# Kernel optimization log

Hardware: AMD Instinct MI355X
Metric: run time of the kernel (lower is better)

The kernel has to match this reference:

```python
import jax, jax.numpy as jnp
import numpy as np

N, DEG, D_IN, D_HID = 50000, 16, 963, 256


def setup_inputs() -> dict:
    key = jax.random.key(0)
    ks = jax.random.split(key, 8)
    s = 0.02
    neighbours = jax.random.randint(ks[0], (N, DEG), 0, N)
    shape_features = jax.random.normal(ks[1], (N, D_IN), dtype=jnp.float32)
    # layer 0: D_IN -> D_HID; layers 1..13 (stacked): D_HID -> D_HID; extra: D_HID -> 3
    W_self0 = jax.random.normal(ks[2], (D_IN, D_HID), dtype=jnp.float32) * s
    W_neigh0 = jax.random.normal(ks[3], (D_IN, D_HID), dtype=jnp.float32) * s
    b0 = jnp.zeros((D_HID,), jnp.float32)
    W_self = jax.random.normal(ks[4], (13, D_HID, D_HID), dtype=jnp.float32) * s
    W_neigh = jax.random.normal(ks[5], (13, D_HID, D_HID), dtype=jnp.float32) * s
    b = jnp.zeros((13, D_HID), jnp.float32)
    W_extra = jax.random.normal(ks[6], (D_HID, 3), dtype=jnp.float32) * s
    b_extra = jnp.zeros((3,), jnp.float32)
    return {
        "neighbours": neighbours,
        "shape_features": shape_features,
        "W_self0": W_self0, "W_neigh0": W_neigh0, "b0": b0,
        "W_self": W_self, "W_neigh": W_neigh, "b": b,
        "W_extra": W_extra, "b_extra": b_extra,
    }


def _gcn(x, neighbours, Ws, Wn, bias):
    # gather neighbour features [N, DEG, D] and sum-aggregate, plus self transform
    agg = jnp.take(x, neighbours, axis=0).sum(axis=1)
    return x @ Ws + agg @ Wn + bias


def reference(neighbours, shape_features, W_self0, W_neigh0, b0, W_self, W_neigh, b, W_extra, b_extra):
    x = jax.nn.relu(_gcn(shape_features, neighbours, W_self0, W_neigh0, b0))
    for i in range(6):  # 6 residual blocks of 2 GCN layers each
        temp = x
        x = jax.nn.relu(_gcn(x, neighbours, W_self[2 * i], W_neigh[2 * i], b[2 * i]))
        x = jax.nn.relu(_gcn(x, neighbours, W_self[2 * i + 1], W_neigh[2 * i + 1], b[2 * i + 1]))
        x = (temp + x) / 2
    x = jax.nn.relu(_gcn(x, neighbours, W_self[12], W_neigh[12], b[12]))
    coordinates = x @ W_extra + b_extra  # extra layer called without neighbours -> linear
    return (x, coordinates)
```

## Files before the change

### kernel.cpp

```cpp
#include <hip/hip_runtime.h>
#include <hip/hip_bf16.h>
#include <hip/hip_fp16.h>
#include <stdint.h>

#define NNODES 50000
#define NPAD   50048
#define DEG    16
#define DIN    963
#define K0PAD  992
#define DHID   256
#define SCALE  (1.0f / 1024.0f)
#define ISCALE 1024.0f

typedef __attribute__((ext_vector_type(4))) float    f32x4;
typedef __attribute__((ext_vector_type(8))) _Float16 f16x8;
typedef __attribute__((ext_vector_type(4))) _Float16 f16x4;

typedef const __attribute__((address_space(1))) void GV;
typedef __attribute__((address_space(3))) void LV;

__device__ __forceinline__ void gl2lds16(const void* g, void* l) {
    __builtin_amdgcn_global_load_lds((GV*)g, (LV*)l, 16, 0, 0);
}

__global__ __launch_bounds__(256) void gemm_dual0(
    const _Float16* __restrict__ A, int K,
    const _Float16* __restrict__ Wp,
    _Float16* __restrict__ ys, _Float16* __restrict__ yn)
{
    __shared__ _Float16 lds[2][2][4096];

    const int tid  = threadIdx.x;
    const int w    = tid >> 6;
    const int lane = tid & 63;
    const int bm   = blockIdx.x * 128;
    const int nb   = blockIdx.y * 128;

    const int KT = K >> 5;

    auto stage = [&](int s, int kt) {
        const int k0 = kt << 5;
#pragma unroll
        for (int i = 0; i < 2; ++i) {
            const int j   = w + (i << 2);
            const int c   = (j << 6) + lane;
            const int row = c & 127;
            const int k8  = (c >> 7) << 3;
            gl2lds16(A  + (size_t)(bm + row) * K + k0 + k8, &lds[s][0][(size_t)j << 9]);
            gl2lds16(Wp + (size_t)(nb + row) * K + k0 + k8, &lds[s][1][(size_t)j << 9]);
        }
    };

    const int wm = (w >> 1) << 6;
    const int wn = (w & 1) << 6;
    const int lr = lane & 15;
    const int kh = lane >> 4;

    f32x4 acc[4][4] = {};

    stage(0, 0);
    __syncthreads();
    int cur = 0;
    for (int kt = 0; kt < KT; ++kt) {
        if (kt + 1 < KT) stage(cur ^ 1, kt + 1);
        f16x8 a[4], b[4];
#pragma unroll
        for (int mi = 0; mi < 4; ++mi)
            a[mi] = *(const f16x8*)&lds[cur][0][((kh << 7) + wm + (mi << 4) + lr) << 3];
#pragma unroll
        for (int ni = 0; ni < 4; ++ni)
            b[ni] = *(const f16x8*)&lds[cur][1][((kh << 7) + wn + (ni << 4) + lr) << 3];
#pragma unroll
        for (int mi = 0; mi < 4; ++mi)
#pragma unroll
            for (int ni = 0; ni < 4; ++ni)
                acc[mi][ni] = __builtin_amdgcn_mfma_f32_16x16x32_f16(a[mi], b[ni], acc[mi][ni], 0, 0, 0);
        __syncthreads();
        cur ^= 1;
    }

    _Float16* C = (blockIdx.y < 2) ? ys : yn;
    const int cb = (nb & 255) + wn;
#pragma unroll
    for (int mi = 0; mi < 4; ++mi) {
        const size_t rbase = (size_t)(bm + wm + (mi << 4) + (kh << 2)) << 8;
#pragma unroll
        for (int ni = 0; ni < 4; ++ni) {
            const int col = cb + (ni << 4) + lr;
#pragma unroll
            for (int r = 0; r < 4; ++r)
                C[rbase + ((size_t)r << 8) + col] = (_Float16)acc[mi][ni][r];
        }
    }
}

template<int FINAL>
__global__ __launch_bounds__(512) void fused_layer(
    const _Float16* __restrict__ X, const int* __restrict__ nbr,
    const _Float16* __restrict__ W, const float* __restrict__ bias,
    const _Float16* __restrict__ res,
    _Float16* __restrict__ outh, float* __restrict__ outf)
{
    __shared__ _Float16 ldsA[2][4096];
    __shared__ _Float16 ldsB[2][8192];

    const int tid  = threadIdx.x;
    const int w    = tid >> 6;
    const int lane = tid & 63;
    const int bm   = blockIdx.x << 7;

    const int growg = bm + (tid >> 2);
    const int nrow  = (growg < NNODES) ? growg : (NNODES - 1);
    const int4* np  = (const int4*)(nbr + nrow * DEG);
    const int4 q0 = np[0], q1 = np[1], q2 = np[2], q3 = np[3];
    const int kq = (tid & 3) << 3;

    auto GLD = [&](int r, int ko) -> f16x8 {
        return *(const f16x8*)(X + ((size_t)r << 8) + ko);
    };
    auto stageAself = [&](int s, int kt) {
        const int c = tid;
        gl2lds16(X + ((size_t)(bm + (c & 127)) << 8) + (kt << 5) + ((c >> 7) << 3),
                 &ldsA[s][(size_t)c << 3]);
    };
    auto stageB = [&](int s, int kt) {
#pragma unroll
        for (int i = 0; i < 2; ++i) {
            const int c = (i << 9) + tid;
            gl2lds16(W + ((size_t)(c & 255) << 9) + (kt << 5) + ((c >> 8) << 3),
                     &ldsB[s][(size_t)c << 3]);
        }
    };

    const int wm = (w >> 2) << 6;
    const int wn = (w & 3) << 6;
    const int lr = lane & 15;
    const int kh = lane >> 4;

    f32x4 acc[4][4] = {};
    f16x8 g0, g1, g2, g3, g4, g5, g6, g7;

    stageAself(0, 0);
    stageB(0, 0);
    __syncthreads();

    int cur = 0;
#pragma unroll
    for (int kt = 0; kt < 16; ++kt) {
        const int nxt = kt + 1;
        if (nxt < 16) {
            if (nxt < 8) {
                stageAself(cur ^ 1, nxt);
            } else {
                const int ko = ((nxt - 8) << 5) + kq;
                g0 = GLD(q0.x, ko); g1 = GLD(q0.y, ko); g2 = GLD(q0.z, ko); g3 = GLD(q0.w, ko);
                g4 = GLD(q1.x, ko); g5 = GLD(q1.y, ko); g6 = GLD(q1.z, ko); g7 = GLD(q1.w, ko);
            }
            stageB(cur ^ 1, nxt);
        }
        f16x8 a[4], b[4];
#pragma unroll
        for (int mi = 0; mi < 4; ++mi)
            a[mi] = *(const f16x8*)&ldsA[cur][((kh << 7) + wm + (mi << 4) + lr) << 3];
#pragma unroll
        for (int ni = 0; ni < 4; ++ni)
            b[ni] = *(const f16x8*)&ldsB[cur][((kh << 8) + wn + (ni << 4) + lr) << 3];
#pragma unroll
        for (int mi = 0; mi < 4; ++mi)
#pragma unroll
            for (int ni = 0; ni < 4; ++ni)
                acc[mi][ni] = __builtin_amdgcn_mfma_f32_16x16x32_f16(a[mi], b[ni], acc[mi][ni], 0, 0, 0);
        if (nxt >= 8 && nxt < 16) {
            const int ko = ((nxt - 8) << 5) + kq;
            f16x8 s0 = ((g0 + g1) + (g2 + g3)) + ((g4 + g5) + (g6 + g7));
            g0 = GLD(q2.x, ko); g1 = GLD(q2.y, ko); g2 = GLD(q2.z, ko); g3 = GLD(q2.w, ko);
            g4 = GLD(q3.x, ko); g5 = GLD(q3.y, ko); g6 = GLD(q3.z, ko); g7 = GLD(q3.w, ko);
            f16x8 s1 = ((g0 + g1) + (g2 + g3)) + ((g4 + g5) + (g6 + g7));
            *(f16x8*)&ldsA[cur ^ 1][(size_t)(((tid & 3) << 7) + (tid >> 2)) << 3] = s0 + s1;
        }
        __syncthreads();
        cur ^= 1;
    }

    const int r0 = kh << 2;
#pragma unroll
    for (int mi = 0; mi < 4; ++mi) {
        const int grow0 = bm + wm + (mi << 4) + r0;
#pragma unroll
        for (int ni = 0; ni < 4; ++ni) {
            const int col = wn + (ni << 4) + lr;
            const float bcol = bias[col] * SCALE;
#pragma unroll
            for (int r = 0; r < 4; ++r) {
                const int grow = grow0 + r;
                float s = acc[mi][ni][r] + bcol;
                s = fmaxf(s, 0.f);
                if (res) s = ((float)res[((size_t)grow << 8) + col] + s) * 0.5f;
                if (FINAL) {
                    if (grow < NNODES) outf[((size_t)grow << 8) + col] = s * ISCALE;
                } else {
                    outh[((size_t)grow << 8) + col] = (_Float16)s;
                }
            }
        }
    }
}

__global__ __launch_bounds__(256) void combine0(
    const _Float16* __restrict__ ys, const _Float16* __restrict__ yn,
    const int* __restrict__ nbr, const float* __restrict__ bias,
    _Float16* __restrict__ outh)
{
    const int w    = threadIdx.x >> 6;
    const int lane = threadIdx.x & 63;
    const int n    = (blockIdx.x << 2) + w;
    const int c4   = lane << 2;
    const size_t base = ((size_t)n << 8) + c4;

    const f16x4 ysv = *(const f16x4*)(ys + base);
    const float4 bv = *(const float4*)(bias + c4);
    float s0 = (float)ysv[0] + bv.x * SCALE;
    float s1 = (float)ysv[1] + bv.y * SCALE;
    float s2 = (float)ysv[2] + bv.z * SCALE;
    float s3 = (float)ysv[3] + bv.w * SCALE;

    const int* nr = nbr + n * DEG;
#pragma unroll
    for (int j = 0; j < DEG; ++j) {
        const f16x4 v = *(const f16x4*)(yn + (((size_t)nr[j]) << 8) + c4);
        s0 += (float)v[0]; s1 += (float)v[1]; s2 += (float)v[2]; s3 += (float)v[3];
    }
    f16x4 o;
    o[0] = (_Float16)fmaxf(s0, 0.f); o[1] = (_Float16)fmaxf(s1, 0.f);
    o[2] = (_Float16)fmaxf(s2, 0.f); o[3] = (_Float16)fmaxf(s3, 0.f);
    *(f16x4*)(outh + base) = o;
}

__global__ __launch_bounds__(64) void coords_kernel(
    const float* __restrict__ x, const float* __restrict__ We,
    const float* __restrict__ be, float* __restrict__ out3, int N)
{
    const int n = blockIdx.x;
    const int l = threadIdx.x;
    const float4 xv = *(const float4*)(x + (size_t)n * 256 + l * 4);
    float p0 = 0.f, p1 = 0.f, p2 = 0.f;
    const float xs[4] = {xv.x, xv.y, xv.z, xv.w};
#pragma unroll
    for (int i = 0; i < 4; ++i) {
        const int cidx = l * 4 + i;
        p0 += xs[i] * We[cidx * 3 + 0];
        p1 += xs[i] * We[cidx * 3 + 1];
        p2 += xs[i] * We[cidx * 3 + 2];
    }
#pragma unroll
    for (int off = 32; off > 0; off >>= 1) {
        p0 += __shfl_down(p0, off);
        p1 += __shfl_down(p1, off);
        p2 += __shfl_down(p2, off);
    }
    if (l == 0) {
        out3[(size_t)n * 3 + 0] = p0 + be[0];
        out3[(size_t)n * 3 + 1] = p1 + be[1];
        out3[(size_t)n * 3 + 2] = p2 + be[2];
    }
}

__global__ __launch_bounds__(256) void conv_sf(const float* __restrict__ sf,
                                               _Float16* __restrict__ sfb)
{
    const int idx = blockIdx.x * 256 + threadIdx.x;
    const int row = idx / 124;
    const int k8  = (idx % 124) << 3;
    f16x8 o = {};
    if (row < NNODES) {
#pragma unroll
        for (int i = 0; i < 8; ++i) {
            const int k = k8 + i;
            o[i] = (k < DIN) ? (_Float16)(sf[(size_t)row * DIN + k] * SCALE) : (_Float16)0.f;
        }
    }
    *(f16x8*)(sfb + (size_t)row * K0PAD + k8) = o;
}

__global__ __launch_bounds__(256) void pack_w0(const float* __restrict__ Ws0,
                                               const float* __restrict__ Wn0,
                                               _Float16* __restrict__ Wp0)
{
    const int idx = blockIdx.x * 256 + threadIdx.x;
    const int nn  = idx & 511;
    const int k8  = idx >> 9;
    const float* W = (nn < 256) ? Ws0 : Wn0;
    const int n0 = nn & 255;
    f16x8 o;
#pragma unroll
    for (int i = 0; i < 8; ++i) {
        const int k = (k8 << 3) + i;
        o[i] = (k < DIN) ? (_Float16)W[(size_t)k * 256 + n0] : (_Float16)0.f;
    }
    *(f16x8*)(Wp0 + (size_t)nn * K0PAD + (k8 << 3)) = o;
}

__global__ __launch_bounds__(256) void pack_w2(const float* __restrict__ Ws,
                                               const float* __restrict__ Wn,
                                               _Float16* __restrict__ Wpk2)
{
    const int idx = blockIdx.x * 256 + threadIdx.x;
    const int n   = idx & 255;
    const int k8  = (idx >> 8) & 63;
    const int l   = idx >> 14;
    f16x8 o;
#pragma unroll
    for (int i = 0; i < 8; ++i) {
        const int k = (k8 << 3) + i;
        const float* W = (k < 256) ? Ws : Wn;
        o[i] = (_Float16)W[(size_t)l * 65536 + (k & 255) * 256 + n];
    }
    *(f16x8*)(Wpk2 + (size_t)l * 131072 + (size_t)n * 512 + (k8 << 3)) = o;
}

extern "C" void kernel_launch(void* const* d_in, const int* in_sizes, int n_in,
                              void* d_out, int out_size, void* d_ws, size_t ws_size,
                              hipStream_t stream)
{
    const int*   nbr = (const int*)d_in[0];
    const float* sf  = (const float*)d_in[1];
    const float* Ws0 = (const float*)d_in[2];
    const float* Wn0 = (const float*)d_in[3];
    const float* b0  = (const float*)d_in[4];
    const float* Ws  = (const float*)d_in[5];
    const float* Wn  = (const float*)d_in[6];
    const float* bb  = (const float*)d_in[7];
    const float* We  = (const float*)d_in[8];
    const float* be  = (const float*)d_in[9];
    float* out = (float*)d_out;

    uint8_t* w = (uint8_t*)d_ws;
    _Float16* sfb  = (_Float16*)w;
    _Float16* P    = (_Float16*)w;
    _Float16* Q    = P + (size_t)NPAD * 256;
    _Float16* Wpk2 = Q + (size_t)NPAD * 256;
    _Float16* Wp0  = (_Float16*)(w + (size_t)NPAD * K0PAD * 2);
    _Float16* ysb  = Wp0 + (size_t)512 * K0PAD;
    _Float16* ynb  = ysb + (size_t)NPAD * 256;

    conv_sf<<<NPAD * 124 / 256, 256, 0, stream>>>(sf, sfb);
    pack_w0<<<512 * 124 / 256, 256, 0, stream>>>(Ws0, Wn0, Wp0);

    gemm_dual0<<<dim3(NPAD / 128, 4), 256, 0, stream>>>(sfb, K0PAD, Wp0, ysb, ynb);
    pack_w2<<<13 * 64 * 256 / 256, 256, 0, stream>>>(Ws, Wn, Wpk2);
    combine0<<<NNODES / 4, 256, 0, stream>>>(ysb, ynb, nbr, b0, P);

    const int fg = NPAD / 128;

    for (int t = 0; t < 6; ++t) {
        const int lA = 2 * t, lB = lA + 1;
        fused_layer<0><<<fg, 512, 0, stream>>>(P, nbr, Wpk2 + (size_t)lA * 131072,
                                               bb + lA * 256, nullptr, Q, nullptr);
        fused_layer<0><<<fg, 512, 0, stream>>>(Q, nbr, Wpk2 + (size_t)lB * 131072,
                                               bb + lB * 256, P, P, nullptr);
    }

    fused_layer<1><<<fg, 512, 0, stream>>>(P, nbr, Wpk2 + (size_t)12 * 131072,
                                           bb + 12 * 256, nullptr, nullptr, out);

    coords_kernel<<<NNODES, 64, 0, stream>>>(out, We, be, out + (size_t)NNODES * 256, NNODES);
}
```

Measured before the change: 1.588 ms.

## Vectorize GEMM epilogues via swapped MFMA operands, XCD-swizzle blocks, widen combine loads

The MFMA operands are swapped so each lane holds four consecutive output columns, which lets the GEMM and fused-layer epilogues do vector f16x4/float4 stores and residual and bias loads instead of scalar ones. The layer-0 GEMM grid is flattened and remapped with an XCD-aware swizzle so neighbouring tiles that share the same A rows land on the same chiplet's L2. The combine kernel now has each thread handle 8 columns with all 16 neighbour gathers issued up front as 16-byte loads. These changes target store and gather efficiency and cache locality, at the cost of higher register pressure in the combine kernel.

```diff
diff --git a/kernel.cpp b/kernel.cpp
--- a/kernel.cpp
+++ b/kernel.cpp
@@ -23,6 +23,11 @@
     __builtin_amdgcn_global_load_lds((GV*)g, (LV*)l, 16, 0, 0);
 }
 
+__device__ __forceinline__ int xcd_swz(int bid, int nwg) {
+    const int q = nwg >> 3, r_ = nwg & 7, xc = bid & 7;
+    return (xc < r_ ? xc * (q + 1) : r_ * (q + 1) + (xc - r_) * q) + (bid >> 3);
+}
+
 __global__ __launch_bounds__(256) void gemm_dual0(
     const _Float16* __restrict__ A, int K,
     const _Float16* __restrict__ Wp,
@@ -33,8 +38,10 @@
     const int tid  = threadIdx.x;
     const int w    = tid >> 6;
     const int lane = tid & 63;
-    const int bm   = blockIdx.x * 128;
-    const int nb   = blockIdx.y * 128;
+
+    const int wgid = xcd_swz(blockIdx.x, gridDim.x);
+    const int bm   = (wgid >> 2) << 7;
+    const int nb   = (wgid & 3) << 7;
 
     const int KT = K >> 5;
 
@@ -74,22 +81,23 @@
         for (int mi = 0; mi < 4; ++mi)
 #pragma unroll
             for (int ni = 0; ni < 4; ++ni)
-                acc[mi][ni] = __builtin_amdgcn_mfma_f32_16x16x32_f16(a[mi], b[ni], acc[mi][ni], 0, 0, 0);
+                acc[mi][ni] = __builtin_amdgcn_mfma_f32_16x16x32_f16(b[ni], a[mi], acc[mi][ni], 0, 0, 0);
         __syncthreads();
         cur ^= 1;
     }
 
-    _Float16* C = (blockIdx.y < 2) ? ys : yn;
+    _Float16* C = (nb < 256) ? ys : yn;
     const int cb = (nb & 255) + wn;
 #pragma unroll
     for (int mi = 0; mi < 4; ++mi) {
-        const size_t rbase = (size_t)(bm + wm + (mi << 4) + (kh << 2)) << 8;
+        const int m = bm + wm + (mi << 4) + lr;
 #pragma unroll
         for (int ni = 0; ni < 4; ++ni) {
-            const int col = cb + (ni << 4) + lr;
-#pragma unroll
-            for (int r = 0; r < 4; ++r)
-                C[rbase + ((size_t)r << 8) + col] = (_Float16)acc[mi][ni][r];
+            const int col0 = cb + (ni << 4) + (kh << 2);
+            f16x4 o;
+#pragma unroll
+            for (int r = 0; r < 4; ++r) o[r] = (_Float16)acc[mi][ni][r];
+            *(f16x4*)(C + ((size_t)m << 8) + col0) = o;
         }
     }
 }
@@ -169,7 +177,7 @@
         for (int mi = 0; mi < 4; ++mi)
 #pragma unroll
             for (int ni = 0; ni < 4; ++ni)
-                acc[mi][ni] = __builtin_amdgcn_mfma_f32_16x16x32_f16(a[mi], b[ni], acc[mi][ni], 0, 0, 0);
+                acc[mi][ni] = __builtin_amdgcn_mfma_f32_16x16x32_f16(b[ni], a[mi], acc[mi][ni], 0, 0, 0);
         if (nxt >= 8 && nxt < 16) {
             const int ko = ((nxt - 8) << 5) + kq;
             f16x8 s0 = ((g0 + g1) + (g2 + g3)) + ((g4 + g5) + (g6 + g7));
@@ -182,58 +190,71 @@
         cur ^= 1;
     }
 
-    const int r0 = kh << 2;
 #pragma unroll
     for (int mi = 0; mi < 4; ++mi) {
-        const int grow0 = bm + wm + (mi << 4) + r0;
+        const int m = bm + wm + (mi << 4) + lr;
+        const size_t mb = (size_t)m << 8;
 #pragma unroll
         for (int ni = 0; ni < 4; ++ni) {
-            const int col = wn + (ni << 4) + lr;
-            const float bcol = bias[col] * SCALE;
-#pragma unroll
-            for (int r = 0; r < 4; ++r) {
-                const int grow = grow0 + r;
-                float s = acc[mi][ni][r] + bcol;
-                s = fmaxf(s, 0.f);
-                if (res) s = ((float)res[((size_t)grow << 8) + col] + s) * 0.5f;
-                if (FINAL) {
-                    if (grow < NNODES) outf[((size_t)grow << 8) + col] = s * ISCALE;
-                } else {
-                    outh[((size_t)grow << 8) + col] = (_Float16)s;
+            const int col0 = wn + (ni << 4) + (kh << 2);
+            const float4 bv = *(const float4*)(bias + col0);
+            float s0 = fmaxf(acc[mi][ni][0] + bv.x * SCALE, 0.f);
+            float s1 = fmaxf(acc[mi][ni][1] + bv.y * SCALE, 0.f);
+            float s2 = fmaxf(acc[mi][ni][2] + bv.z * SCALE, 0.f);
+            float s3 = fmaxf(acc[mi][ni][3] + bv.w * SCALE, 0.f);
+            if (res) {
+                const f16x4 rv = *(const f16x4*)(res + mb + col0);
+                s0 = ((float)rv[0] + s0) * 0.5f;
+                s1 = ((float)rv[1] + s1) * 0.5f;
+                s2 = ((float)rv[2] + s2) * 0.5f;
+                s3 = ((float)rv[3] + s3) * 0.5f;
+            }
+            if (FINAL) {
+                if (m < NNODES) {
+                    float4 o = make_float4(s0 * ISCALE, s1 * ISCALE, s2 * ISCALE, s3 * ISCALE);
+                    *(float4*)(outf + mb + col0) = o;
                 }
+            } else {
+                f16x4 o;
+                o[0] = (_Float16)s0; o[1] = (_Float16)s1;
+                o[2] = (_Float16)s2; o[3] = (_Float16)s3;
+                *(f16x4*)(outh + mb + col0) = o;
             }
         }
     }
 }
 
-__global__ __launch_bounds__(256) void combine0(
+__global__ __launch_bounds__(256) void combine16(
     const _Float16* __restrict__ ys, const _Float16* __restrict__ yn,
     const int* __restrict__ nbr, const float* __restrict__ bias,
     _Float16* __restrict__ outh)
 {
-    const int w    = threadIdx.x >> 6;
-    const int lane = threadIdx.x & 63;
-    const int n    = (blockIdx.x << 2) + w;
-    const int c4   = lane << 2;
-    const size_t base = ((size_t)n << 8) + c4;
-
-    const f16x4 ysv = *(const f16x4*)(ys + base);
-    const float4 bv = *(const float4*)(bias + c4);
-    float s0 = (float)ysv[0] + bv.x * SCALE;
-    float s1 = (float)ysv[1] + bv.y * SCALE;
-    float s2 = (float)ysv[2] + bv.z * SCALE;
-    float s3 = (float)ysv[3] + bv.w * SCALE;
-
-    const int* nr = nbr + n * DEG;
-#pragma unroll
-    for (int j = 0; j < DEG; ++j) {
-        const f16x4 v = *(const f16x4*)(yn + (((size_t)nr[j]) << 8) + c4);
-        s0 += (float)v[0]; s1 += (float)v[1]; s2 += (float)v[2]; s3 += (float)v[3];
-    }
-    f16x4 o;
-    o[0] = (_Float16)fmaxf(s0, 0.f); o[1] = (_Float16)fmaxf(s1, 0.f);
-    o[2] = (_Float16)fmaxf(s2, 0.f); o[3] = (_Float16)fmaxf(s3, 0.f);
-    *(f16x4*)(outh + base) = o;
+    const int idx = blockIdx.x * 256 + threadIdx.x;
+    const int r   = idx >> 5;
+    const int c8  = (idx & 31) << 3;
+    const int4* np = (const int4*)(nbr + r * DEG);
+    const int4 q0 = np[0], q1 = np[1], q2 = np[2], q3 = np[3];
+
+    f16x8 v[16];
+#define LD16(slot, n) v[slot] = *(const f16x8*)(yn + ((size_t)(n) << 8) + c8)
+    LD16(0,  q0.x); LD16(1,  q0.y); LD16(2,  q0.z); LD16(3,  q0.w);
+    LD16(4,  q1.x); LD16(5,  q1.y); LD16(6,  q1.z); LD16(7,  q1.w);
+    LD16(8,  q2.x); LD16(9,  q2.y); LD16(10, q2.z); LD16(11, q2.w);
+    LD16(12, q3.x); LD16(13, q3.y); LD16(14, q3.z); LD16(15, q3.w);
+#undef LD16
+    const f16x8 ysv = *(const f16x8*)(ys + ((size_t)r << 8) + c8);
+    const float4 b0 = *(const float4*)(bias + c8);
+    const float4 b1 = *(const float4*)(bias + c8 + 4);
+    const float bb[8] = {b0.x, b0.y, b0.z, b0.w, b1.x, b1.y, b1.z, b1.w};
+    f16x8 o;
+#pragma unroll
+    for (int i = 0; i < 8; ++i) {
+        float s = (float)ysv[i] + bb[i] * SCALE;
+#pragma unroll
+        for (int j = 0; j < 16; ++j) s += (float)v[j][i];
+        o[i] = (_Float16)fmaxf(s, 0.f);
+    }
+    *(f16x8*)(outh + ((size_t)r << 8) + c8) = o;
 }
 
 __global__ __launch_bounds__(64) void coords_kernel(
@@ -346,9 +367,9 @@
     conv_sf<<<NPAD * 124 / 256, 256, 0, stream>>>(sf, sfb);
     pack_w0<<<512 * 124 / 256, 256, 0, stream>>>(Ws0, Wn0, Wp0);
 
-    gemm_dual0<<<dim3(NPAD / 128, 4), 256, 0, stream>>>(sfb, K0PAD, Wp0, ysb, ynb);
+    gemm_dual0<<<(NPAD / 128) * 4, 256, 0, stream>>>(sfb, K0PAD, Wp0, ysb, ynb);
     pack_w2<<<13 * 64 * 256 / 256, 256, 0, stream>>>(Ws, Wn, Wpk2);
-    combine0<<<NNODES / 4, 256, 0, stream>>>(ysb, ynb, nbr, b0, P);
+    combine16<<<NNODES * 32 / 256, 256, 0, stream>>>(ysb, ynb, nbr, b0, P);
 
     const int fg = NPAD / 128;
 
```

Measured after the change: 1.546 ms. 1.03x faster.
